# Kernel tuning notes

Measured on AMD Instinct MI355X. Metric: run time of the kernel, lower is better.

## Reference

```python
import jax, jax.numpy as jnp
import numpy as np

K = 3  # kernel size per dim
PAD = K // 2
CHANS = [1, 40, 80, 160, 80, 40, 1]  # channel ladder of the 6 convNd layers


def conv4d(x, w, b):
    """4D convolution, stride 1, 'same' padding.
    x: [B, Cin, D1, D2, D3, D4]; w: [Cout, Cin, K, K, K, K]; b: [Cout].
    Implemented as K shifted 3D convs along D1 (D1 folded into batch), summed.
    """
    B, Cin, D1, D2, D3, D4 = x.shape
    Cout = w.shape[0]
    # pad only D1 here; the inner conv pads D2..D4
    xp = jnp.pad(x, ((0, 0), (0, 0), (PAD, PAD), (0, 0), (0, 0), (0, 0)))
    xp = jnp.transpose(xp, (0, 2, 1, 3, 4, 5))  # [B, D1+2p, Cin, D2, D3, D4]
    dn = jax.lax.conv_dimension_numbers(
        (B * D1, Cin, D2, D3, D4), (Cout, Cin, K, K, K),
        ('NCDHW', 'OIDHW', 'NCDHW'))
    acc = None
    for i in range(K):  # small fixed loop over kernel taps along D1
        xs = xp[:, i:i + D1].reshape(B * D1, Cin, D2, D3, D4)
        y = jax.lax.conv_general_dilated(
            xs, w[:, :, i], window_strides=(1, 1, 1),
            padding=[(PAD, PAD)] * 3, dimension_numbers=dn)
        acc = y if acc is None else acc + y
    out = acc.reshape(B, D1, Cout, D2, D3, D4)
    out = jnp.transpose(out, (0, 2, 1, 3, 4, 5))
    return out + b[None, :, None, None, None, None]


def setup_inputs() -> dict:
    key = jax.random.key(0)
    kx, key = jax.random.split(key)
    inp = {'x': jax.random.normal(kx, (2, 1, 16, 16, 16, 16), dtype=jnp.float32)}
    for l in range(6):
        kw, key = jax.random.split(key)
        cin, cout = CHANS[l], CHANS[l + 1]
        std = (2.0 / (cin * K ** 4)) ** 0.5  # Kaiming-style fan-in init
        inp[f'w{l + 1}'] = jax.random.normal(kw, (cout, cin, K, K, K, K), dtype=jnp.float32) * std
        inp[f'b{l + 1}'] = jnp.zeros((cout,), dtype=jnp.float32)
    return inp


def reference(x, w1, b1, w2, b2, w3, b3, w4, b4, w5, b5, w6, b6):
    h = jax.nn.relu(conv4d(x, w1, b1))
    h = jax.nn.relu(conv4d(h, w2, b2))
    h = jax.nn.relu(conv4d(h, w3, b3))
    h = jax.nn.relu(conv4d(h, w4, b4))
    h = jax.nn.relu(conv4d(h, w5, b5))
    h = conv4d(h, w6, b6)
    return jax.nn.relu(h)
```

## Files before the change

### kernel.cpp

```cpp
#include <hip/hip_runtime.h>

typedef __attribute__((ext_vector_type(8))) short short8;
typedef __attribute__((ext_vector_type(4))) float f32x4;

__device__ __forceinline__ ushort f2bf(float f){
    union { float f; unsigned u; } v; v.f = f;
    unsigned r = (v.u + 0x7fffu + ((v.u >> 16) & 1u)) >> 16;
    return (ushort)r;
}
__device__ __forceinline__ float bf2f(ushort u){
    union { unsigned u; float f; } v; v.u = ((unsigned)u) << 16;
    return v.f;
}

__global__ __launch_bounds__(256) void conv_l1(
    const float* __restrict__ x, const float* __restrict__ w,
    const float* __restrict__ bias, ushort* __restrict__ out)
{
    __shared__ float xs[2916];
    __shared__ float wsh[3240];
    const int tid = threadIdx.x;
    const int bx = blockIdx.x;
    const int d2 = bx & 15, d1 = (bx >> 4) & 15, b = bx >> 8;
    const float* xb = x + (size_t)b * 65536;

    for (int i = tid; i < 2916; i += 256){
        int i4 = i % 18; int r1 = i / 18; int i3 = r1 % 18;
        int r2 = r1 / 18; int a2 = r2 % 3; int a1 = r2 / 3;
        int e1 = d1 + a1 - 1, e2 = d2 + a2 - 1, e3 = i3 - 1, e4 = i4 - 1;
        float v = 0.f;
        if ((unsigned)e1 < 16u && (unsigned)e2 < 16u && (unsigned)e3 < 16u && (unsigned)e4 < 16u)
            v = xb[((e1 * 16 + e2) * 16 + e3) * 16 + e4];
        xs[i] = v;
    }
    for (int i = tid; i < 3240; i += 256) wsh[i] = w[i];
    __syncthreads();

    const int d3 = tid >> 4, d4 = tid & 15;
    float acc[40];
    #pragma unroll
    for (int c = 0; c < 40; ++c) acc[c] = 0.f;

    for (int t1 = 0; t1 < 3; ++t1)
    for (int t2 = 0; t2 < 3; ++t2)
    for (int t3 = 0; t3 < 3; ++t3)
    #pragma unroll
    for (int t4 = 0; t4 < 3; ++t4){
        float xv = xs[((t1 * 3 + t2) * 18 + d3 + t3) * 18 + d4 + t4];
        int tap = ((t1 * 3 + t2) * 3 + t3) * 3 + t4;
        #pragma unroll
        for (int c = 0; c < 40; ++c) acc[c] += wsh[c * 81 + tap] * xv;
    }

    ushort* ob = out + ((size_t)bx * 256 + tid) * 64;
    #pragma unroll
    for (int c = 0; c < 40; ++c){
        float v = acc[c] + bias[c]; v = v > 0.f ? v : 0.f;
        ob[c] = f2bf(v);
    }
    #pragma unroll
    for (int c = 40; c < 64; ++c) ob[c] = 0;
}

__global__ __launch_bounds__(256) void conv_l6(
    const ushort* __restrict__ in, const float* __restrict__ w,
    const float* __restrict__ bias, float* __restrict__ out)
{
    __shared__ float wsh[3240];
    const int tid = threadIdx.x;
    const int bx = blockIdx.x;
    const int d2 = bx & 15, d1 = (bx >> 4) & 15, b = bx >> 8;
    for (int i = tid; i < 3240; i += 256) wsh[i] = w[i];
    __syncthreads();

    const int d3 = tid >> 4, d4 = tid & 15;
    const ushort* inb = in + (size_t)b * 65536 * 48;
    float acc = 0.f;
    for (int t1 = 0; t1 < 3; ++t1){
        int e1 = d1 + t1 - 1; if ((unsigned)e1 >= 16u) continue;
        for (int t2 = 0; t2 < 3; ++t2){
            int e2 = d2 + t2 - 1; if ((unsigned)e2 >= 16u) continue;
            for (int t3 = 0; t3 < 3; ++t3){
                int e3 = d3 + t3 - 1; if ((unsigned)e3 >= 16u) continue;
                for (int t4 = 0; t4 < 3; ++t4){
                    int e4 = d4 + t4 - 1; if ((unsigned)e4 >= 16u) continue;
                    const ushort* p = inb + (size_t)(((e1 * 16 + e2) * 16 + e3) * 16 + e4) * 48;
                    int tap = ((t1 * 3 + t2) * 3 + t3) * 3 + t4;
                    #pragma unroll
                    for (int c8 = 0; c8 < 5; ++c8){
                        short8 v = *(const short8*)(p + c8 * 8);
                        #pragma unroll
                        for (int j = 0; j < 8; ++j)
                            acc += bf2f((ushort)v[j]) * wsh[(c8 * 8 + j) * 81 + tap];
                    }
                }
            }
        }
    }
    float v = acc + bias[0]; v = v > 0.f ? v : 0.f;
    out[(size_t)bx * 256 + tid] = v;
}

__global__ void repack_wq(const float* __restrict__ w, ushort* __restrict__ wq,
                          int cin_real, int cout_real, int kc, int cout_w, int nstrip)
{
    const int ncc = 27 * kc;
    const int total = nstrip * ncc * 8192;
    for (int o = blockIdx.x * blockDim.x + threadIdx.x; o < total; o += gridDim.x * blockDim.x){
        const int j = o & 7;
        const int u = (o >> 3) & 1023;
        const int chunk = o >> 13;
        const int strip = chunk / ncc;
        const int cc = chunk - strip * ncc;
        const int gg = cc / (kc * 3);
        const int rem = cc - gg * (kc * 3);
        const int kh = rem / 3;
        const int t3 = rem - kh * 3;
        float v = 0.f;
        if (u < 12 * cout_w){
            const int per = 4 * cout_w;
            const int t4 = u / per;
            const int rest = u - t4 * per;
            const int gk = rest / cout_w;
            const int col = rest - gk * cout_w;
            const int tap = gg * 9 + t3 * 3 + t4;
            const int ci = kh * 32 + gk * 8 + j;
            const int co = strip * cout_w + col;
            if (ci < cin_real && co < cout_real)
                v = w[((size_t)co * cin_real + ci) * 81 + tap];
        }
        wq[o] = f2bf(v);
    }
}

template<int CIN_S, int COUT_W, int OST, int CREAL, int PADC>
__global__ __launch_bounds__(256, 3) void conv16(
    const ushort* __restrict__ in, const ushort* __restrict__ wq,
    const float* __restrict__ bias, ushort* __restrict__ out)
{
    constexpr int KC  = CIN_S / 32;
    constexpr int NT  = COUT_W / 16;
    constexpr int NCC = 27 * KC;
    constexpr int AH  = 18 * 18 * 32;

    __shared__ __attribute__((aligned(16))) ushort As[2][AH];

    const int tid  = threadIdx.x;
    const int lane = tid & 63;
    const int wm   = tid >> 6;
    const int r    = lane & 15;
    const int g    = lane >> 4;

    const int p0 = blockIdx.x;
    const int strip = p0 >> 9;
    const int pp = p0 & 511;
    const int bx = (pp & 7) * 64 + (pp >> 3);
    const int d2 = bx & 15, d1 = (bx >> 4) & 15, b = bx >> 8;
    const int co_base = strip * COUT_W;

    const ushort* inb = in + (size_t)b * 65536 * CIN_S;
    const ushort* wqs = wq + ((size_t)strip * NCC << 13);

    unsigned long long gpack = 0ull; int ng = 0;
    #pragma unroll
    for (int gg = 0; gg < 9; ++gg){
        const int t1 = gg / 3, t2 = gg - (gg / 3) * 3;
        if ((unsigned)(d1 + t1 - 1) < 16u && (unsigned)(d2 + t2 - 1) < 16u){
            gpack |= ((unsigned long long)gg) << (ng * 4);
            ++ng;
        }
    }
    const int nchunk = ng * KC;

    f32x4 acc[4][NT];
    #pragma unroll
    for (int mi = 0; mi < 4; ++mi)
        #pragma unroll
        for (int n = 0; n < NT; ++n)
            acc[mi][n] = (f32x4){0.f, 0.f, 0.f, 0.f};

    short8 areg[4];
    const int e4s = lane >> 2;
    const int jl  = lane & 3;
    const int gcs = jl ^ ((lane >> 3) & 3);

    auto loadAreg = [&](int c){
        const int gi = c / KC, kh = c - gi * KC;
        const int gg = (int)((gpack >> (gi * 4)) & 15ull);
        const int t1 = gg / 3, t2 = gg - t1 * 3;
        const ushort* src = inb + ((size_t)((d1 + t1 - 1) * 16 + (d2 + t2 - 1)) * 256) * CIN_S + kh * 32;
        #pragma unroll
        for (int k = 0; k < 4; ++k){
            const int row = wm * 4 + k;
            areg[k] = *(const short8*)(src + (size_t)(row * 16 + e4s) * CIN_S + gcs * 8);
        }
    };
    auto writeA = [&](ushort* dst){
        #pragma unroll
        for (int k = 0; k < 4; ++k){
            const int row = wm * 4 + k;
            *(short8*)(dst + ((row + 1) * 18 + 1 + e4s) * 32 + jl * 8) = areg[k];
        }
    };

    {
        const short8 z = {0, 0, 0, 0, 0, 0, 0, 0};
        short8* a0 = (short8*)As[0];
        short8* a1 = (short8*)As[1];
        for (int i = tid; i < AH / 8; i += 256){ a0[i] = z; a1[i] = z; }
    }
    asm volatile("s_waitcnt lgkmcnt(0)" ::: "memory");
    __builtin_amdgcn_s_barrier();
    loadAreg(0);
    writeA(As[0]);
    if (nchunk > 1) loadAreg(1);
    asm volatile("s_waitcnt lgkmcnt(0)" ::: "memory");
    __builtin_amdgcn_s_barrier();

    for (int c = 0; c < nchunk; ++c){
        if (c + 1 < nchunk) writeA(As[(c + 1) & 1]);

        const int gi = c / KC, kh = c - gi * KC;
        const int gg = (int)((gpack >> (gi * 4)) & 15ull);
        const ushort* Ab = As[c & 1];
        const ushort* Bg0 = wqs + ((size_t)((gg * KC + kh) * 3) << 13);

        #pragma unroll
        for (int t3 = 0; t3 < 3; ++t3){
            if (t3 == 1 && c + 2 < nchunk) loadAreg(c + 2);
            const ushort* Bg = Bg0 + ((size_t)t3 << 13);
            __builtin_amdgcn_s_setprio(1);
            #pragma unroll
            for (int t4 = 0; t4 < 3; ++t4){
                const int e4 = r + t4 - 1;
                const int gsw = (g ^ ((e4 >> 1) & 3)) * 8;
                const ushort* arow = Ab + ((wm * 4 + t3) * 18 + (e4 + 1)) * 32 + gsw;
                short8 bfr[NT];
                #pragma unroll
                for (int n = 0; n < NT; ++n)
                    bfr[n] = *(const short8*)(Bg + ((t4 * 4 + g) * COUT_W + n * 16 + r) * 8);
                #pragma unroll
                for (int mi = 0; mi < 4; ++mi){
                    const short8 af = *(const short8*)(arow + mi * (18 * 32));
                    #pragma unroll
                    for (int n = 0; n < NT; ++n)
                        acc[mi][n] = __builtin_amdgcn_mfma_f32_16x16x32_bf16(af, bfr[n], acc[mi][n], 0, 0, 0);
                }
            }
            __builtin_amdgcn_s_setprio(0);
        }

        asm volatile("s_waitcnt lgkmcnt(0)" ::: "memory");
        __builtin_amdgcn_s_barrier();
    }

    float bv[NT];
    #pragma unroll
    for (int n = 0; n < NT; ++n){
        const int co = co_base + n * 16 + r;
        bv[n] = (co < CREAL) ? bias[co] : 0.f;
    }
    ushort* ob = out + (size_t)bx * 256 * OST;
    #pragma unroll
    for (int mi = 0; mi < 4; ++mi){
        #pragma unroll
        for (int n = 0; n < NT; ++n){
            const int co = co_base + n * 16 + r;
            #pragma unroll
            for (int j = 0; j < 4; ++j){
                const int row = 64 * wm + 16 * mi + g * 4 + j;
                float v = acc[mi][n][j] + bv[n];
                v = v > 0.f ? v : 0.f;
                ob[(size_t)row * OST + co] = f2bf(v);
            }
        }
    }
    if (PADC > 0){
        const int row = 64 * wm + lane;
        const short8 z = {0, 0, 0, 0, 0, 0, 0, 0};
        #pragma unroll
        for (int pc = 0; pc < PADC; pc += 8)
            *(short8*)(ob + (size_t)row * OST + CREAL + pc) = z;
    }
}

extern "C" void kernel_launch(void* const* d_in, const int* in_sizes, int n_in,
                              void* d_out, int out_size, void* d_ws, size_t ws_size,
                              hipStream_t stream) {
    const float* x  = (const float*)d_in[0];
    const float* w1 = (const float*)d_in[1];  const float* b1 = (const float*)d_in[2];
    const float* w2 = (const float*)d_in[3];  const float* b2 = (const float*)d_in[4];
    const float* w3 = (const float*)d_in[5];  const float* b3 = (const float*)d_in[6];
    const float* w4 = (const float*)d_in[7];  const float* b4 = (const float*)d_in[8];
    const float* w5 = (const float*)d_in[9];  const float* b5 = (const float*)d_in[10];
    const float* w6 = (const float*)d_in[11]; const float* b6 = (const float*)d_in[12];

    ushort* bufA = (ushort*)d_ws;
    ushort* bufB = bufA + (size_t)131072 * 160;
    ushort* wq2  = bufB + (size_t)131072 * 96;
    ushort* wq3  = wq2 + (size_t)54  * 8192;
    ushort* wq4  = wq3 + (size_t)162 * 8192;
    ushort* wq5  = wq4 + (size_t)135 * 8192;

    repack_wq<<<512, 256, 0, stream>>>(w2, wq2,  40,  80, 2, 80, 1);
    repack_wq<<<512, 256, 0, stream>>>(w3, wq3,  80, 160, 3, 80, 2);
    repack_wq<<<512, 256, 0, stream>>>(w4, wq4, 160,  80, 5, 80, 1);
    repack_wq<<<512, 256, 0, stream>>>(w5, wq5,  80,  40, 3, 48, 1);

    conv_l1<<<512, 256, 0, stream>>>(x, w1, b1, bufA);
    conv16<  64,   80,  96,  80,  16><<< 512, 256, 0, stream>>>(bufA, wq2, b2, bufB);
    conv16<  96,   80, 160, 160,   0><<<1024, 256, 0, stream>>>(bufB, wq3, b3, bufA);
    conv16< 160,   80,  96,  80,  16><<< 512, 256, 0, stream>>>(bufA, wq4, b4, bufB);
    conv16<  96,   48,  48,  40,   0><<< 512, 256, 0, stream>>>(bufB, wq5, b5, bufA);
    conv_l6<<<512, 256, 0, stream>>>(bufA, w6, b6, (float*)d_out);
}
```

Before: 885.3 us.

## Stage weights in LDS via async loads and split output channels across waves

The conv16 kernels now run 512 threads with 8 waves, split into 4 along M and 2 along output channels. Weight tiles are copied into double-buffered LDS with global_load_lds instead of being read from global memory per wave. The A tile shrinks to a single 16-row buffer whose halo is handled by predication, and the repacked weights use a compact XOR-swizzled layout to avoid LDS bank conflicts. This should cut redundant global weight traffic and raise MFMA occupancy, but adds more barriers per chunk and uneven N work when NT is odd.

```diff
diff --git a/kernel.cpp b/kernel.cpp
--- a/kernel.cpp
+++ b/kernel.cpp
@@ -2,6 +2,10 @@
 
 typedef __attribute__((ext_vector_type(8))) short short8;
 typedef __attribute__((ext_vector_type(4))) float f32x4;
+
+#define GLD16(gsrc, ldst) __builtin_amdgcn_global_load_lds( \
+    (const __attribute__((address_space(1))) unsigned int*)(gsrc), \
+    (__attribute__((address_space(3))) unsigned int*)(ldst), 16, 0, 0)
 
 __device__ __forceinline__ ushort f2bf(float f){
     union { float f; unsigned u; } v; v.f = f;
@@ -105,51 +109,60 @@
                           int cin_real, int cout_real, int kc, int cout_w, int nstrip)
 {
     const int ncc = 27 * kc;
-    const int total = nstrip * ncc * 8192;
+    const int upc = 12 * cout_w;
+    const int total = nstrip * ncc * upc * 8;
     for (int o = blockIdx.x * blockDim.x + threadIdx.x; o < total; o += gridDim.x * blockDim.x){
         const int j = o & 7;
-        const int u = (o >> 3) & 1023;
-        const int chunk = o >> 13;
-        const int strip = chunk / ncc;
-        const int cc = chunk - strip * ncc;
+        const int t = o >> 3;
+        const int u_phys = t % upc;
+        const int chunkT = t / upc;
+        const int strip = chunkT / ncc;
+        const int cc = chunkT - strip * ncc;
         const int gg = cc / (kc * 3);
         const int rem = cc - gg * (kc * 3);
         const int kh = rem / 3;
         const int t3 = rem - kh * 3;
+        const int per = 4 * cout_w;
+        const int gk = (u_phys % per) / cout_w;
+        const int u = u_phys ^ gk;
+        const int t4 = u / per;
+        const int rest = u - t4 * per;
+        const int gk2 = rest / cout_w;
+        const int col = rest - gk2 * cout_w;
+        const int tap = gg * 9 + t3 * 3 + t4;
+        const int ci = kh * 32 + gk2 * 8 + j;
+        const int co = strip * cout_w + col;
         float v = 0.f;
-        if (u < 12 * cout_w){
-            const int per = 4 * cout_w;
-            const int t4 = u / per;
-            const int rest = u - t4 * per;
-            const int gk = rest / cout_w;
-            const int col = rest - gk * cout_w;
-            const int tap = gg * 9 + t3 * 3 + t4;
-            const int ci = kh * 32 + gk * 8 + j;
-            const int co = strip * cout_w + col;
-            if (ci < cin_real && co < cout_real)
-                v = w[((size_t)co * cin_real + ci) * 81 + tap];
-        }
+        if (ci < cin_real && co < cout_real)
+            v = w[((size_t)co * cin_real + ci) * 81 + tap];
         wq[o] = f2bf(v);
     }
 }
 
 template<int CIN_S, int COUT_W, int OST, int CREAL, int PADC>
-__global__ __launch_bounds__(256, 3) void conv16(
+__global__ __launch_bounds__(512, 4) void conv16(
     const ushort* __restrict__ in, const ushort* __restrict__ wq,
     const float* __restrict__ bias, ushort* __restrict__ out)
 {
     constexpr int KC  = CIN_S / 32;
-    constexpr int NT  = COUT_W / 16;
+    constexpr int NTT = COUT_W / 16;
+    constexpr int NT0 = (NTT + 1) / 2;
+    constexpr int NT1 = NTT - NT0;
     constexpr int NCC = 27 * KC;
-    constexpr int AH  = 18 * 18 * 32;
-
-    __shared__ __attribute__((aligned(16))) ushort As[2][AH];
+    constexpr int B8U = 12 * COUT_W;
+
+    __shared__ __attribute__((aligned(16))) ushort As[16 * 18 * 32];
+    __shared__ __attribute__((aligned(16))) ushort Bs[2][B8U * 8];
 
     const int tid  = threadIdx.x;
     const int lane = tid & 63;
-    const int wm   = tid >> 6;
+    const int wv   = tid >> 6;
+    const int wm   = wv >> 1;
+    const int wn   = wv & 1;
     const int r    = lane & 15;
     const int g    = lane >> 4;
+    const int ntw  = wn ? NT1 : NT0;
+    const int co0  = wn ? NT0 * 16 : 0;
 
     const int p0 = blockIdx.x;
     const int strip = p0 >> 9;
@@ -159,7 +172,7 @@
     const int co_base = strip * COUT_W;
 
     const ushort* inb = in + (size_t)b * 65536 * CIN_S;
-    const ushort* wqs = wq + ((size_t)strip * NCC << 13);
+    const ushort* wqs = wq + (size_t)strip * NCC * B8U * 8;
 
     unsigned long long gpack = 0ull; int ng = 0;
     #pragma unroll
@@ -172,17 +185,14 @@
     }
     const int nchunk = ng * KC;
 
-    f32x4 acc[4][NT];
+    f32x4 acc[4][NT0];
     #pragma unroll
     for (int mi = 0; mi < 4; ++mi)
         #pragma unroll
-        for (int n = 0; n < NT; ++n)
+        for (int n = 0; n < NT0; ++n)
             acc[mi][n] = (f32x4){0.f, 0.f, 0.f, 0.f};
 
-    short8 areg[4];
-    const int e4s = lane >> 2;
-    const int jl  = lane & 3;
-    const int gcs = jl ^ ((lane >> 3) & 3);
+    short8 areg[2];
 
     auto loadAreg = [&](int c){
         const int gi = c / KC, kh = c - gi * KC;
@@ -190,92 +200,120 @@
         const int t1 = gg / 3, t2 = gg - t1 * 3;
         const ushort* src = inb + ((size_t)((d1 + t1 - 1) * 16 + (d2 + t2 - 1)) * 256) * CIN_S + kh * 32;
         #pragma unroll
-        for (int k = 0; k < 4; ++k){
-            const int row = wm * 4 + k;
-            areg[k] = *(const short8*)(src + (size_t)(row * 16 + e4s) * CIN_S + gcs * 8);
+        for (int k = 0; k < 2; ++k){
+            const int u = k * 512 + tid;
+            const int pos = u >> 2, gc = u & 3;
+            const int e4s = pos & 15;
+            const int gcs = gc ^ ((e4s >> 1) & 3);
+            areg[k] = *(const short8*)(src + (size_t)pos * CIN_S + gcs * 8);
         }
     };
-    auto writeA = [&](ushort* dst){
-        #pragma unroll
-        for (int k = 0; k < 4; ++k){
-            const int row = wm * 4 + k;
-            *(short8*)(dst + ((row + 1) * 18 + 1 + e4s) * 32 + jl * 8) = areg[k];
+    auto writeA = [&](){
+        #pragma unroll
+        for (int k = 0; k < 2; ++k){
+            const int u = k * 512 + tid;
+            const int pos = u >> 2, gc = u & 3;
+            const int e3 = pos >> 4, e4s = pos & 15;
+            *(short8*)(As + (e3 * 18 + e4s + 1) * 32 + gc * 8) = areg[k];
         }
     };
-
-    {
+    auto issueB = [&](int sg){
+        const int cc = sg / 3, tt = sg - cc * 3;
+        const int gi = cc / KC, kh = cc - gi * KC;
+        const int gg = (int)((gpack >> (gi * 4)) & 15ull);
+        const ushort* src = wqs + (size_t)((gg * KC + kh) * 3 + tt) * B8U * 8;
+        ushort* dst = Bs[sg & 1];
+        #pragma unroll
+        for (int k = 0; k < 2; ++k){
+            const int u0 = k * 512 + wv * 64;
+            if (u0 < B8U)
+                GLD16(src + (size_t)(u0 + lane) * 8, dst + u0 * 8);
+        }
+    };
+
+    if (tid < 128){
+        const int e3z = tid >> 3, side = (tid >> 2) & 1, gz = tid & 3;
         const short8 z = {0, 0, 0, 0, 0, 0, 0, 0};
-        short8* a0 = (short8*)As[0];
-        short8* a1 = (short8*)As[1];
-        for (int i = tid; i < AH / 8; i += 256){ a0[i] = z; a1[i] = z; }
-    }
+        *(short8*)(As + (e3z * 18 + side * 17) * 32 + gz * 8) = z;
+    }
+    loadAreg(0);
+    writeA();
+    issueB(0);
     asm volatile("s_waitcnt lgkmcnt(0)" ::: "memory");
-    __builtin_amdgcn_s_barrier();
-    loadAreg(0);
-    writeA(As[0]);
-    if (nchunk > 1) loadAreg(1);
-    asm volatile("s_waitcnt lgkmcnt(0)" ::: "memory");
-    __builtin_amdgcn_s_barrier();
 
     for (int c = 0; c < nchunk; ++c){
-        if (c + 1 < nchunk) writeA(As[(c + 1) & 1]);
-
-        const int gi = c / KC, kh = c - gi * KC;
-        const int gg = (int)((gpack >> (gi * 4)) & 15ull);
-        const ushort* Ab = As[c & 1];
-        const ushort* Bg0 = wqs + ((size_t)((gg * KC + kh) * 3) << 13);
-
+        const int s0 = c * 3;
         #pragma unroll
         for (int t3 = 0; t3 < 3; ++t3){
-            if (t3 == 1 && c + 2 < nchunk) loadAreg(c + 2);
-            const ushort* Bg = Bg0 + ((size_t)t3 << 13);
+            const int s = s0 + t3;
+            if (t3 == 2 && c + 1 < nchunk)
+                asm volatile("s_waitcnt vmcnt(2)" ::: "memory");
+            else
+                asm volatile("s_waitcnt vmcnt(0)" ::: "memory");
+            __builtin_amdgcn_s_barrier();
+            __builtin_amdgcn_sched_barrier(0);
+
+            if (s + 1 < nchunk * 3) issueB(s + 1);
+            if (t3 == 1 && c + 1 < nchunk) loadAreg(c + 1);
+
+            const ushort* Bb = Bs[s & 1];
             __builtin_amdgcn_s_setprio(1);
             #pragma unroll
             for (int t4 = 0; t4 < 3; ++t4){
                 const int e4 = r + t4 - 1;
                 const int gsw = (g ^ ((e4 >> 1) & 3)) * 8;
-                const ushort* arow = Ab + ((wm * 4 + t3) * 18 + (e4 + 1)) * 32 + gsw;
-                short8 bfr[NT];
+                short8 bfr[NT0];
                 #pragma unroll
-                for (int n = 0; n < NT; ++n)
-                    bfr[n] = *(const short8*)(Bg + ((t4 * 4 + g) * COUT_W + n * 16 + r) * 8);
+                for (int n = 0; n < NT0; ++n)
+                    if (n < NT1 || wn == 0)
+                        bfr[n] = *(const short8*)(Bb + ((((t4 * 4 + g) * COUT_W + co0 + n * 16 + r) * 8) ^ (g << 3)));
                 #pragma unroll
                 for (int mi = 0; mi < 4; ++mi){
-                    const short8 af = *(const short8*)(arow + mi * (18 * 32));
-                    #pragma unroll
-                    for (int n = 0; n < NT; ++n)
-                        acc[mi][n] = __builtin_amdgcn_mfma_f32_16x16x32_bf16(af, bfr[n], acc[mi][n], 0, 0, 0);
+                    const int e3 = 4 * wm + mi + t3 - 1;
+                    if ((unsigned)e3 < 16u){
+                        const short8 af = *(const short8*)(As + (e3 * 18 + e4 + 1) * 32 + gsw);
+                        #pragma unroll
+                        for (int n = 0; n < NT0; ++n)
+                            if (n < NT1 || wn == 0)
+                                acc[mi][n] = __builtin_amdgcn_mfma_f32_16x16x32_bf16(af, bfr[n], acc[mi][n], 0, 0, 0);
+                    }
                 }
             }
             __builtin_amdgcn_s_setprio(0);
         }
 
-        asm volatile("s_waitcnt lgkmcnt(0)" ::: "memory");
-        __builtin_amdgcn_s_barrier();
-    }
-
-    float bv[NT];
-    #pragma unroll
-    for (int n = 0; n < NT; ++n){
-        const int co = co_base + n * 16 + r;
+        if (c + 1 < nchunk){
+            __builtin_amdgcn_sched_barrier(0);
+            __builtin_amdgcn_s_barrier();
+            writeA();
+            asm volatile("s_waitcnt lgkmcnt(0)" ::: "memory");
+        }
+    }
+
+    float bv[NT0];
+    #pragma unroll
+    for (int n = 0; n < NT0; ++n){
+        const int co = co_base + co0 + n * 16 + r;
         bv[n] = (co < CREAL) ? bias[co] : 0.f;
     }
     ushort* ob = out + (size_t)bx * 256 * OST;
     #pragma unroll
     for (int mi = 0; mi < 4; ++mi){
         #pragma unroll
-        for (int n = 0; n < NT; ++n){
-            const int co = co_base + n * 16 + r;
-            #pragma unroll
-            for (int j = 0; j < 4; ++j){
-                const int row = 64 * wm + 16 * mi + g * 4 + j;
-                float v = acc[mi][n][j] + bv[n];
-                v = v > 0.f ? v : 0.f;
-                ob[(size_t)row * OST + co] = f2bf(v);
+        for (int n = 0; n < NT0; ++n){
+            if (n < NT1 || wn == 0){
+                const int co = co_base + co0 + n * 16 + r;
+                #pragma unroll
+                for (int j = 0; j < 4; ++j){
+                    const int row = 64 * wm + 16 * mi + g * 4 + j;
+                    float v = acc[mi][n][j] + bv[n];
+                    v = v > 0.f ? v : 0.f;
+                    ob[(size_t)row * OST + co] = f2bf(v);
+                }
             }
         }
     }
-    if (PADC > 0){
+    if (PADC > 0 && wn == 0){
         const int row = 64 * wm + lane;
         const short8 z = {0, 0, 0, 0, 0, 0, 0, 0};
         #pragma unroll
@@ -298,9 +336,9 @@
     ushort* bufA = (ushort*)d_ws;
     ushort* bufB = bufA + (size_t)131072 * 160;
     ushort* wq2  = bufB + (size_t)131072 * 96;
-    ushort* wq3  = wq2 + (size_t)54  * 8192;
-    ushort* wq4  = wq3 + (size_t)162 * 8192;
-    ushort* wq5  = wq4 + (size_t)135 * 8192;
+    ushort* wq3  = wq2 + (size_t)54  * 7680;
+    ushort* wq4  = wq3 + (size_t)162 * 7680;
+    ushort* wq5  = wq4 + (size_t)135 * 7680;
 
     repack_wq<<<512, 256, 0, stream>>>(w2, wq2,  40,  80, 2, 80, 1);
     repack_wq<<<512, 256, 0, stream>>>(w3, wq3,  80, 160, 3, 80, 2);
@@ -308,9 +346,9 @@
     repack_wq<<<512, 256, 0, stream>>>(w5, wq5,  80,  40, 3, 48, 1);
 
     conv_l1<<<512, 256, 0, stream>>>(x, w1, b1, bufA);
-    conv16<  64,   80,  96,  80,  16><<< 512, 256, 0, stream>>>(bufA, wq2, b2, bufB);
-    conv16<  96,   80, 160, 160,   0><<<1024, 256, 0, stream>>>(bufB, wq3, b3, bufA);
-    conv16< 160,   80,  96,  80,  16><<< 512, 256, 0, stream>>>(bufA, wq4, b4, bufB);
-    conv16<  96,   48,  48,  40,   0><<< 512, 256, 0, stream>>>(bufB, wq5, b5, bufA);
+    conv16<  64,   80,  96,  80,  16><<< 512, 512, 0, stream>>>(bufA, wq2, b2, bufB);
+    conv16<  96,   80, 160, 160,   0><<<1024, 512, 0, stream>>>(bufB, wq3, b3, bufA);
+    conv16< 160,   80,  96,  80,  16><<< 512, 512, 0, stream>>>(bufA, wq4, b4, bufB);
+    conv16<  96,   48,  48,  40,   0><<< 512, 512, 0, stream>>>(bufB, wq5, b5, bufA);
     conv_l6<<<512, 256, 0, stream>>>(bufA, w6, b6, (float*)d_out);
 }
```

Result: slower. 915.7 us (+3.4%).
